# Kernel optimization log

Hardware: AMD Instinct MI355X
Metric: run time of the kernel (lower is better)

Reference implementation:

```python
import math
import jax, jax.numpy as jnp
import numpy as np

SDE_THRESHOLD = 10.0
ANGLE_THRESHOLD_DEG = 30.0


def setup_inputs() -> dict:
    key = jax.random.key(0)
    k1, k2 = jax.random.split(key)
    B, H, N = 8, 16, 1024
    y_pred = jax.random.normal(k1, (B, H, 4), dtype=jnp.float32)
    sample_points = jax.random.normal(k2, (B, N, 3), dtype=jnp.float32)
    return {"y_pred": y_pred, "sample_points": sample_points}


def reference(y_pred, sample_points):
    # y_pred: [B,H,4] = (nx,ny,nz,d) per plane head; sample_points: [B,N,3]
    B, H, _ = y_pred.shape
    n = y_pred[..., :3]
    n = n / jnp.linalg.norm(n, axis=-1, keepdims=True)  # normalize normals
    d = y_pred[..., 3]

    # transform_representation_cm: represent plane by (normal, point) where
    # point = projection of the point-cloud centroid onto the plane n.x + d = 0
    cm = sample_points.mean(axis=1)  # [B,3]
    point = cm[:, None, :] - (jnp.einsum('bhd,bd->bh', n, cm) + d)[..., None] * n  # [B,H,3]

    # chamfer_adapter: reflect points across each plane, bidirectional chamfer (squared dists)
    proj = jnp.einsum('bnd,bhd->bhn', sample_points, n) + d[:, :, None]  # [B,H,N]
    refl = sample_points[:, None, :, :] - 2.0 * proj[..., None] * n[:, :, None, :]  # [B,H,N,3]
    rr = jnp.sum(refl * refl, axis=-1)                  # [B,H,N]
    ss = jnp.sum(sample_points * sample_points, axis=-1)  # [B,N]
    cross = jnp.einsum('bhid,bjd->bhij', refl, sample_points)  # [B,H,N,N]
    d2 = rr[..., None] + ss[:, None, None, :] - 2.0 * cross
    sde = jnp.min(d2, axis=-1).mean(axis=-1) + jnp.min(d2, axis=-2).mean(axis=-1)  # [B,H]

    # minmax_normalization -> confidence = 1 - (sde - min) / |max - min| per batch row
    mn = sde.min(axis=1, keepdims=True)
    mx = sde.max(axis=1, keepdims=True)
    conf = 1.0 - (sde - mn) / jnp.abs(mx - mn)

    # pairwise angle-based duplicate suppression (vectorized NMS)
    cos = jnp.clip(jnp.einsum('bhd,bgd->bhg', n, n), -1.0, 1.0)
    ang = jnp.arccos(cos) * (180.0 / math.pi)
    close = (ang < ANGLE_THRESHOLD_DEG) | (180.0 - ang < ANGLE_THRESHOLD_DEG)
    close = close & ~jnp.eye(H, dtype=bool)
    valid = sde <= SDE_THRESHOLD  # filter x.sde <= sde_threshold
    # plane i is popped iff exists valid j (close) with sde_i >= sde_j (equal sde pops both)
    sup = valid & jnp.any(close & valid[:, None, :] & (sde[:, :, None] >= sde[:, None, :]), axis=-1)
    keep = valid & ~sup

    # to_tensor(): [normal(3), point(3), confidence, sde]; sort kept by confidence desc,
    # zero-pad suppressed/filtered slots (fixed shape [B,H,8] instead of ragged pad_sequence)
    planes = jnp.concatenate([n, point, conf[..., None], sde[..., None]], axis=-1)  # [B,H,8]
    sort_key = jnp.where(keep, conf, -jnp.inf)
    order = jnp.argsort(-sort_key, axis=1)
    planes_s = jnp.take_along_axis(planes, order[..., None], axis=1)
    keep_s = jnp.take_along_axis(keep, order, axis=1)
    return jnp.where(keep_s[..., None], planes_s, 0.0)
```

## Files before the change

kernel.cpp:

```cpp
#include <hip/hip_runtime.h>
#include <math.h>

#define BB 8
#define HH 16
#define NN 1024
#define TB 256
#define POWN 4
#define NSC 4
#define SCH 256


__global__ __launch_bounds__(TB) void chamfer_kernel(
    const float* __restrict__ y_pred,
    const float* __restrict__ sp,
    float* __restrict__ ws)
{
    __shared__ __align__(16) float4 pts[SCH];

    const int blk = blockIdx.x;
    const int bh  = blk >> 2;
    const int sc  = blk & (NSC - 1);
    const int b   = bh >> 4;
    const int tid = threadIdx.x;

    float pnx = y_pred[bh * 4 + 0];
    float pny = y_pred[bh * 4 + 1];
    float pnz = y_pred[bh * 4 + 2];
    float pd  = y_pred[bh * 4 + 3];
    float inv = 1.0f / sqrtf(pnx * pnx + pny * pny + pnz * pnz);
    pnx *= inv; pny *= inv; pnz *= inv;

    const float* spb = sp + (size_t)b * NN * 3;

    {
        int j = sc * SCH + tid;
        float x = spb[j * 3 + 0], y = spb[j * 3 + 1], z = spb[j * 3 + 2];
        pts[tid] = make_float4(x, y, z, x * x + y * y + z * z);
    }

    float mx[POWN], my[POWN], mz[POWN], osq[POWN];
#pragma unroll
    for (int u = 0; u < POWN; ++u) {
        int i = u * TB + tid;
        float x = spb[i * 3 + 0], y = spb[i * 3 + 1], z = spb[i * 3 + 2];
        float proj = x * pnx + y * pny + z * pnz + pd;
        x -= 2.0f * proj * pnx;
        y -= 2.0f * proj * pny;
        z -= 2.0f * proj * pnz;
        osq[u] = x * x + y * y + z * z;
        mx[u] = -2.0f * x; my[u] = -2.0f * y; mz[u] = -2.0f * z;
    }
    __syncthreads();

    float m0[POWN], m1[POWN];
#pragma unroll
    for (int u = 0; u < POWN; ++u) { m0[u] = 3.4e38f; m1[u] = 3.4e38f; }

#define DIST(q, u) fmaf(mx[u], q.x, fmaf(my[u], q.y, fmaf(mz[u], q.z, q.w)))
#define STEP4 do { \
    _Pragma("unroll") \
    for (int u = 0; u < POWN; ++u) { \
        float da = DIST(qa, u); \
        float db = DIST(qb, u); \
        float dc = DIST(qc, u); \
        float dd = DIST(qd, u); \
        m0[u] = fminf(fminf(m0[u], da), db); \
        m1[u] = fminf(fminf(m1[u], dc), dd); \
    } } while (0)

    float4 qa = pts[0], qb = pts[1], qc = pts[2], qd = pts[3];
    for (int j = 0; j < SCH - 4; j += 4) {
        float4 na = pts[j + 4];
        float4 nb = pts[j + 5];
        float4 nc = pts[j + 6];
        float4 nd = pts[j + 7];
        STEP4;
        qa = na; qb = nb; qc = nc; qd = nd;
    }
    STEP4;

#undef STEP4
#undef DIST

    float* wp = ws + (size_t)(bh * NSC + sc) * NN;
#pragma unroll
    for (int u = 0; u < POWN; ++u)
        wp[u * TB + tid] = osq[u] + fminf(m0[u], m1[u]);
}

__global__ __launch_bounds__(TB) void finalize_kernel(
    const float* __restrict__ ws,
    const float* __restrict__ y_pred,
    const float* __restrict__ sp,
    float* __restrict__ out)
{
    const int b   = blockIdx.x;
    const int tid = threadIdx.x;

    __shared__ float sde_s[HH], nx_s[HH], ny_s[HH], nz_s[HH], d_s[HH], conf_s[HH];
    __shared__ float cmacc[3];
    __shared__ int keep_s[HH];

    if (tid < HH) sde_s[tid] = 0.0f;
    if (tid < 3)  cmacc[tid] = 0.0f;
    __syncthreads();

    const float* spb = sp + (size_t)b * NN * 3;
    float sx = 0.0f, sy = 0.0f, sz = 0.0f;
    for (int p = tid; p < NN; p += TB) {
        sx += spb[p * 3 + 0];
        sy += spb[p * 3 + 1];
        sz += spb[p * 3 + 2];
    }
    for (int off = 32; off; off >>= 1) {
        sx += __shfl_down(sx, off, 64);
        sy += __shfl_down(sy, off, 64);
        sz += __shfl_down(sz, off, 64);
    }
    if ((tid & 63) == 0) {
        atomicAdd(&cmacc[0], sx);
        atomicAdd(&cmacc[1], sy);
        atomicAdd(&cmacc[2], sz);
    }

    {
        const int h   = tid >> 4;
        const int sub = tid & 15;
        const float* base = ws + (size_t)((b * HH + h) * NSC) * NN;
        const float4* q0 = (const float4*)(base);
        const float4* q1 = (const float4*)(base + NN);
        const float4* q2 = (const float4*)(base + 2 * NN);
        const float4* q3 = (const float4*)(base + 3 * NN);
        float acc = 0.0f;
        for (int g = 0; g < 16; ++g) {
            int i4 = sub * 16 + g;
            float4 a0 = q0[i4], a1 = q1[i4], a2 = q2[i4], a3 = q3[i4];
            float e0 = fminf(fminf(a0.x, a1.x), fminf(a2.x, a3.x));
            float e1 = fminf(fminf(a0.y, a1.y), fminf(a2.y, a3.y));
            float e2 = fminf(fminf(a0.z, a1.z), fminf(a2.z, a3.z));
            float e3 = fminf(fminf(a0.w, a1.w), fminf(a2.w, a3.w));
            acc += (e0 + e1) + (e2 + e3);
        }
        atomicAdd(&sde_s[h], acc);
    }
    __syncthreads();

    const float cmx = cmacc[0] / NN, cmy = cmacc[1] / NN, cmz = cmacc[2] / NN;

    if (tid < HH) {
        int h = tid;
        float nx = y_pred[(b * HH + h) * 4 + 0];
        float ny = y_pred[(b * HH + h) * 4 + 1];
        float nz = y_pred[(b * HH + h) * 4 + 2];
        float d  = y_pred[(b * HH + h) * 4 + 3];
        float inv = 1.0f / sqrtf(nx * nx + ny * ny + nz * nz);
        nx *= inv; ny *= inv; nz *= inv;
        nx_s[h] = nx; ny_s[h] = ny; nz_s[h] = nz; d_s[h] = d;
        sde_s[h] = sde_s[h] * (2.0f / NN);
    }
    __syncthreads();

    if (tid < HH) {
        int h = tid;
        float mn = sde_s[0], mx = sde_s[0];
        for (int g = 1; g < HH; ++g) {
            mn = fminf(mn, sde_s[g]);
            mx = fmaxf(mx, sde_s[g]);
        }
        float sde  = sde_s[h];
        float conf = 1.0f - (sde - mn) / fabsf(mx - mn);
        conf_s[h]  = conf;
        bool valid = (sde <= 10.0f);
        bool sup   = false;
        if (valid) {
            for (int g = 0; g < HH; ++g) {
                if (g == h) continue;
                float c = nx_s[h] * nx_s[g] + ny_s[h] * ny_s[g] + nz_s[h] * nz_s[g];
                c = fminf(1.0f, fmaxf(-1.0f, c));
                float ang = acosf(c) * 57.29577951308232f;
                bool close = (ang < 30.0f) || (180.0f - ang < 30.0f);
                if (close && (sde_s[g] <= 10.0f) && (sde >= sde_s[g])) sup = true;
            }
        }
        keep_s[h] = (valid && !sup) ? 1 : 0;
    }
    __syncthreads();

    if (tid < HH) {
        int h = tid;
        float keyh = keep_s[h] ? conf_s[h] : -INFINITY;
        int pos = 0;
        for (int g = 0; g < HH; ++g) {
            float keyg = keep_s[g] ? conf_s[g] : -INFINITY;
            if (keyg > keyh || (keyg == keyh && g < h)) ++pos;
        }
        float nx = nx_s[h], ny = ny_s[h], nz = nz_s[h];
        float t  = nx * cmx + ny * cmy + nz * cmz + d_s[h];
        float px = cmx - t * nx, py = cmy - t * ny, pz = cmz - t * nz;

        float* o = out + (size_t)(b * HH + pos) * 8;
        if (keep_s[h]) {
            o[0] = nx; o[1] = ny; o[2] = nz;
            o[3] = px; o[4] = py; o[5] = pz;
            o[6] = conf_s[h];
            o[7] = sde_s[h];
        } else {
            for (int c = 0; c < 8; ++c) o[c] = 0.0f;
        }
    }
}

extern "C" void kernel_launch(void* const* d_in, const int* in_sizes, int n_in,
                              void* d_out, int out_size, void* d_ws, size_t ws_size,
                              hipStream_t stream) {
    const float* y_pred = (const float*)d_in[0];
    const float* sp     = (const float*)d_in[1];
    float* out          = (float*)d_out;
    float* ws           = (float*)d_ws;

    chamfer_kernel<<<dim3(BB * HH * NSC), dim3(TB), 0, stream>>>(y_pred, sp, ws);
    finalize_kernel<<<dim3(BB), dim3(TB), 0, stream>>>(ws, y_pred, sp, out);
}
```

Baseline: 83.18 us.

## Move chamfer partial-min reduction into a separate wide reduce kernel

Adds a reduce kernel with one block per (batch, head). Each block takes the min over the four chunk partials and sums them into a per-plane total stored in the workspace. Before, the single-block-per-batch finalize kernel did all of this, so only 8 blocks read about 2 MB. The chamfer inner loop also drops its manual register prefetch in favour of a plain 4-point unrolled loop. The cost is an extra kernel launch and a round trip through global memory.

```diff
diff --git a/kernel.cpp b/kernel.cpp
--- a/kernel.cpp
+++ b/kernel.cpp
@@ -5,9 +5,10 @@
 #define HH 16
 #define NN 1024
 #define TB 256
-#define POWN 4
 #define NSC 4
 #define SCH 256
+#define POWN 4
+#define SUMBASE (BB * HH * NSC * NN)
 
 
 __global__ __launch_bounds__(TB) void chamfer_kernel(
@@ -30,7 +31,7 @@
     float inv = 1.0f / sqrtf(pnx * pnx + pny * pny + pnz * pnz);
     pnx *= inv; pny *= inv; pnz *= inv;
 
-    const float* spb = sp + (size_t)b * NN * 3;
+    const float* __restrict__ spb = sp + (size_t)b * NN * 3;
 
     {
         int j = sc * SCH + tid;
@@ -56,36 +57,55 @@
 #pragma unroll
     for (int u = 0; u < POWN; ++u) { m0[u] = 3.4e38f; m1[u] = 3.4e38f; }
 
-#define DIST(q, u) fmaf(mx[u], q.x, fmaf(my[u], q.y, fmaf(mz[u], q.z, q.w)))
-#define STEP4 do { \
-    _Pragma("unroll") \
-    for (int u = 0; u < POWN; ++u) { \
-        float da = DIST(qa, u); \
-        float db = DIST(qb, u); \
-        float dc = DIST(qc, u); \
-        float dd = DIST(qd, u); \
-        m0[u] = fminf(fminf(m0[u], da), db); \
-        m1[u] = fminf(fminf(m1[u], dc), dd); \
-    } } while (0)
-
-    float4 qa = pts[0], qb = pts[1], qc = pts[2], qd = pts[3];
-    for (int j = 0; j < SCH - 4; j += 4) {
-        float4 na = pts[j + 4];
-        float4 nb = pts[j + 5];
-        float4 nc = pts[j + 6];
-        float4 nd = pts[j + 7];
-        STEP4;
-        qa = na; qb = nb; qc = nc; qd = nd;
-    }
-    STEP4;
-
-#undef STEP4
+#define DIST(qq, u) fmaf(mx[u], qq.x, fmaf(my[u], qq.y, fmaf(mz[u], qq.z, qq.w)))
+    for (int j = 0; j < SCH; j += 4) {
+        float4 q0 = pts[j + 0];
+        float4 q1 = pts[j + 1];
+        float4 q2 = pts[j + 2];
+        float4 q3 = pts[j + 3];
+#pragma unroll
+        for (int u = 0; u < POWN; ++u) {
+            float d0 = DIST(q0, u);
+            float d1 = DIST(q1, u);
+            float d2 = DIST(q2, u);
+            float d3 = DIST(q3, u);
+            m0[u] = fminf(fminf(m0[u], d0), d1);
+            m1[u] = fminf(fminf(m1[u], d2), d3);
+        }
+    }
 #undef DIST
 
     float* wp = ws + (size_t)(bh * NSC + sc) * NN;
 #pragma unroll
     for (int u = 0; u < POWN; ++u)
         wp[u * TB + tid] = osq[u] + fminf(m0[u], m1[u]);
+}
+
+__global__ __launch_bounds__(TB) void reduce_kernel(
+    const float* __restrict__ ws_in,
+    float* __restrict__ ws_out)
+{
+    __shared__ float wsum[4];
+    const int bh  = blockIdx.x;
+    const int tid = threadIdx.x;
+
+    const float4* r0 = (const float4*)(ws_in + (size_t)(bh * NSC + 0) * NN);
+    const float4* r1 = (const float4*)(ws_in + (size_t)(bh * NSC + 1) * NN);
+    const float4* r2 = (const float4*)(ws_in + (size_t)(bh * NSC + 2) * NN);
+    const float4* r3 = (const float4*)(ws_in + (size_t)(bh * NSC + 3) * NN);
+
+    float4 a0 = r0[tid], a1 = r1[tid], a2 = r2[tid], a3 = r3[tid];
+    float e0 = fminf(fminf(a0.x, a1.x), fminf(a2.x, a3.x));
+    float e1 = fminf(fminf(a0.y, a1.y), fminf(a2.y, a3.y));
+    float e2 = fminf(fminf(a0.z, a1.z), fminf(a2.z, a3.z));
+    float e3 = fminf(fminf(a0.w, a1.w), fminf(a2.w, a3.w));
+    float s  = (e0 + e1) + (e2 + e3);
+
+    for (int off = 32; off; off >>= 1) s += __shfl_down(s, off, 64);
+    if ((tid & 63) == 0) wsum[tid >> 6] = s;
+    __syncthreads();
+    if (tid == 0)
+        ws_out[SUMBASE + bh] = (wsum[0] + wsum[1]) + (wsum[2] + wsum[3]);
 }
 
 __global__ __launch_bounds__(TB) void finalize_kernel(
@@ -101,8 +121,7 @@
     __shared__ float cmacc[3];
     __shared__ int keep_s[HH];
 
-    if (tid < HH) sde_s[tid] = 0.0f;
-    if (tid < 3)  cmacc[tid] = 0.0f;
+    if (tid < 3) cmacc[tid] = 0.0f;
     __syncthreads();
 
     const float* spb = sp + (size_t)b * NN * 3;
@@ -121,27 +140,6 @@
         atomicAdd(&cmacc[0], sx);
         atomicAdd(&cmacc[1], sy);
         atomicAdd(&cmacc[2], sz);
-    }
-
-    {
-        const int h   = tid >> 4;
-        const int sub = tid & 15;
-        const float* base = ws + (size_t)((b * HH + h) * NSC) * NN;
-        const float4* q0 = (const float4*)(base);
-        const float4* q1 = (const float4*)(base + NN);
-        const float4* q2 = (const float4*)(base + 2 * NN);
-        const float4* q3 = (const float4*)(base + 3 * NN);
-        float acc = 0.0f;
-        for (int g = 0; g < 16; ++g) {
-            int i4 = sub * 16 + g;
-            float4 a0 = q0[i4], a1 = q1[i4], a2 = q2[i4], a3 = q3[i4];
-            float e0 = fminf(fminf(a0.x, a1.x), fminf(a2.x, a3.x));
-            float e1 = fminf(fminf(a0.y, a1.y), fminf(a2.y, a3.y));
-            float e2 = fminf(fminf(a0.z, a1.z), fminf(a2.z, a3.z));
-            float e3 = fminf(fminf(a0.w, a1.w), fminf(a2.w, a3.w));
-            acc += (e0 + e1) + (e2 + e3);
-        }
-        atomicAdd(&sde_s[h], acc);
     }
     __syncthreads();
 
@@ -156,7 +154,7 @@
         float inv = 1.0f / sqrtf(nx * nx + ny * ny + nz * nz);
         nx *= inv; ny *= inv; nz *= inv;
         nx_s[h] = nx; ny_s[h] = ny; nz_s[h] = nz; d_s[h] = d;
-        sde_s[h] = sde_s[h] * (2.0f / NN);
+        sde_s[h] = ws[SUMBASE + b * HH + h] * (2.0f / NN);
     }
     __syncthreads();
 
@@ -219,5 +217,6 @@
     float* ws           = (float*)d_ws;
 
     chamfer_kernel<<<dim3(BB * HH * NSC), dim3(TB), 0, stream>>>(y_pred, sp, ws);
+    reduce_kernel<<<dim3(BB * HH), dim3(TB), 0, stream>>>(ws, ws);
     finalize_kernel<<<dim3(BB), dim3(TB), 0, stream>>>(ws, y_pred, sp, out);
 }
```

Result: faster. 75.40 us (-9.4%).
